# Performance work log

Hardware: AMD Instinct MI355X
Metric: run time of the kernel (lower is better)

Reference implementation:

```python
import jax, jax.numpy as jnp
import numpy as np

RPN_BATCHSIZE = 256
RPN_FG_FRACTION = 0.5
NEG_OVERLAP = 0.3
POS_OVERLAP = 0.7
STRIDE = 16
ALLOWED_BORDER = 0.0


def _whctrs(a):
    w = a[2] - a[0] + 1.0
    h = a[3] - a[1] + 1.0
    return w, h, a[0] + 0.5 * (w - 1.0), a[1] + 0.5 * (h - 1.0)


def _mkanchors(ws, hs, xc, yc):
    return np.stack([xc - 0.5 * (ws - 1.0), yc - 0.5 * (hs - 1.0),
                     xc + 0.5 * (ws - 1.0), yc + 0.5 * (hs - 1.0)], axis=1)


def _base_anchors(base_size=16, ratios=(0.5, 1.0, 2.0), scales=(8.0, 16.0, 32.0)):
    ratios = np.asarray(ratios, np.float64)
    scales = np.asarray(scales, np.float64)
    base = np.array([1.0, 1.0, base_size, base_size]) - 1.0
    w, h, xc, yc = _whctrs(base)
    size = w * h
    ws = np.round(np.sqrt(size / ratios))
    hs = np.round(ws * ratios)
    ratio_anchors = _mkanchors(ws, hs, xc, yc)
    out = []
    for ra in ratio_anchors:
        w2, h2, xc2, yc2 = _whctrs(ra)
        out.append(_mkanchors(w2 * scales, h2 * scales, xc2, yc2))
    return np.concatenate(out, axis=0).astype(np.float32)  # (9, 4)


def _shift_anchors(rr, cc, stride):
    base = jnp.asarray(_base_anchors())  # (9, 4)
    sx = jnp.arange(rr, dtype=jnp.float32) * stride
    sy = jnp.arange(cc, dtype=jnp.float32) * stride
    SX, SY = jnp.meshgrid(sx, sy)  # 'xy' indexing like keras meshgrid
    shifts = jnp.stack([SX.ravel(), SY.ravel(), SX.ravel(), SY.ravel()], axis=1)
    return (base[None, :, :] + shifts[:, None, :]).reshape(-1, 4)  # (rr*cc*9, 4)


def _overlap(a, b):
    # pairwise IoU with the +1 pixel convention of keras_rcnn.backend.overlap
    area_a = (a[:, 2] - a[:, 0] + 1.0) * (a[:, 3] - a[:, 1] + 1.0)  # (N,)
    area_b = (b[:, 2] - b[:, 0] + 1.0) * (b[:, 3] - b[:, 1] + 1.0)  # (G,)
    iw = jnp.maximum(jnp.minimum(a[:, None, 2], b[None, :, 2]) - jnp.maximum(a[:, None, 0], b[None, :, 0]) + 1.0, 0.0)
    ih = jnp.maximum(jnp.minimum(a[:, None, 3], b[None, :, 3]) - jnp.maximum(a[:, None, 1], b[None, :, 1]) + 1.0, 0.0)
    inter = iw * ih
    return inter / (area_a[:, None] + area_b[None, :] - inter)


def _subsample(labels, target_value, max_count, key):
    # Randomly demote entries with labels == target_value beyond max_count to -1.
    # Replaces the TF shuffle+scatter with a vectorized rank-based selection.
    is_t = labels == target_value
    pri = jnp.where(is_t, jax.random.uniform(key, labels.shape), -1.0)
    order = jnp.argsort(-pri)
    n = labels.shape[0]
    rank = jnp.zeros((n,), jnp.int32).at[order].set(jnp.arange(n, dtype=jnp.int32))
    drop = is_t & (rank >= max_count)
    return jnp.where(drop, -1.0, labels)


def _bbox_transform(ex, gt):
    ew = ex[:, 2] - ex[:, 0] + 1.0
    eh = ex[:, 3] - ex[:, 1] + 1.0
    ecx = ex[:, 0] + 0.5 * ew
    ecy = ex[:, 1] + 0.5 * eh
    gw = gt[:, 2] - gt[:, 0] + 1.0
    gh = gt[:, 3] - gt[:, 1] + 1.0
    gcx = gt[:, 0] + 0.5 * gw
    gcy = gt[:, 1] + 0.5 * gh
    dx = (gcx - ecx) / ew
    dy = (gcy - ecy) / eh
    dw = jnp.log(gw / ew)
    dh = jnp.log(gh / eh)
    return jnp.stack([dx, dy, dw, dh], axis=1)


def _forward(scores, gt_boxes, metadata):
    meta = metadata[0]
    gt = gt_boxes[0]
    rr, cc = scores.shape[1], scores.shape[2]
    anchors = _shift_anchors(rr, cc, STRIDE)
    n = anchors.shape[0]
    iou = _overlap(anchors, gt)  # (N, G), dominant memory traffic
    argmax_inds = jnp.argmax(iou, axis=1)        # best gt per anchor
    max_overlaps = jnp.max(iou, axis=1)
    gt_argmax_inds = jnp.argmax(iou, axis=0)     # best anchor per gt
    labels = jnp.full((n,), -1.0, jnp.float32)
    labels = jnp.where(max_overlaps < NEG_OVERLAP, 0.0, labels)
    # unique+scatter_add in the original just sets those positions to 1
    labels = labels.at[gt_argmax_inds].set(1.0)
    labels = jnp.where(max_overlaps >= POS_OVERLAP, 1.0, labels)
    kpos, kneg = jax.random.split(jax.random.key(42))
    num_fg = int(RPN_FG_FRACTION * RPN_BATCHSIZE)
    labels = _subsample(labels, 1.0, num_fg, kpos)
    num_bg = RPN_BATCHSIZE - jnp.sum(labels == 1.0)
    labels = _subsample(labels, 0.0, num_bg, kneg)
    gt_sel = gt[argmax_inds]  # (N, 4)
    targets = _bbox_transform(anchors, gt_sel)
    inside = ((anchors[:, 0] >= -ALLOWED_BORDER) & (anchors[:, 1] >= -ALLOWED_BORDER) &
              (anchors[:, 2] < ALLOWED_BORDER + meta[1]) & (anchors[:, 3] < ALLOWED_BORDER + meta[0]))
    labels = jnp.where(inside, labels, -1.0)
    return labels[None, :], targets[None, :, :]


def setup_inputs() -> dict:
    key = jax.random.key(0)
    k1, k2 = jax.random.split(key)
    rr = cc = 128
    num_anchors = 9
    g = 256
    scores = jnp.zeros((1, rr, cc, 2 * num_anchors), jnp.float32)
    xy1 = jax.random.uniform(k1, (g, 2), jnp.float32) * 1600.0
    wh = 32.0 + jax.random.uniform(k2, (g, 2), jnp.float32) * 416.0
    xy2 = jnp.minimum(xy1 + wh, 2047.0)
    gt_boxes = jnp.concatenate([xy1, xy2], axis=1)[None, :, :]
    metadata = jnp.array([[2048.0, 2048.0, 1.0]], jnp.float32)
    return {"scores": scores, "gt_boxes": gt_boxes, "metadata": metadata}


def reference(scores, gt_boxes, metadata):
    return _forward(scores, gt_boxes, metadata)
```

## Files before the change

kernel.cpp:

```cpp
#include <hip/hip_runtime.h>
#include <stdint.h>

#pragma clang fp contract(off)

#define N_ANCH 147456
#define HALF_N 73728u
#define NG 256
#define NBINS 4096
#define CAND_CAP 4096
#define K_POS 128u
#define RPN_BATCH 256u
#define PARTITIONABLE 1

struct TFOut { uint32_t x0, x1; };

__host__ __device__ constexpr TFOut threefry2x32(uint32_t k0, uint32_t k1,
                                                 uint32_t c0, uint32_t c1) {
  uint32_t ks[3] = {k0, k1, k0 ^ k1 ^ 0x1BD11BDAu};
  uint32_t x0 = c0 + ks[0];
  uint32_t x1 = c1 + ks[1];
  const uint32_t rotA[4] = {13u, 15u, 26u, 6u};
  const uint32_t rotB[4] = {17u, 29u, 16u, 24u};
#pragma unroll
  for (int g = 0; g < 5; ++g) {
#pragma unroll
    for (int r = 0; r < 4; ++r) {
      uint32_t ro = ((g & 1) == 0) ? rotA[r] : rotB[r];
      x0 += x1;
      x1 = (x1 << ro) | (x1 >> (32u - ro));
      x1 ^= x0;
    }
    x0 += ks[(g + 1) % 3];
    x1 += ks[(g + 2) % 3] + (uint32_t)(g + 1);
  }
  return TFOut{x0, x1};
}

#if PARTITIONABLE
constexpr TFOut SK0 = threefry2x32(0u, 42u, 0u, 0u);
constexpr TFOut SK1 = threefry2x32(0u, 42u, 0u, 1u);
constexpr uint32_t KPOS0 = SK0.x0, KPOS1 = SK0.x1;
constexpr uint32_t KNEG0 = SK1.x0, KNEG1 = SK1.x1;
#else
constexpr TFOut SA = threefry2x32(0u, 42u, 0u, 2u);
constexpr TFOut SB = threefry2x32(0u, 42u, 1u, 3u);
constexpr uint32_t KPOS0 = SA.x0, KPOS1 = SB.x0;
constexpr uint32_t KNEG0 = SA.x1, KNEG1 = SB.x1;
#endif

__device__ __forceinline__ uint32_t rand_m23(uint32_t k0, uint32_t k1, uint32_t i) {
#if PARTITIONABLE
  TFOut o = threefry2x32(k0, k1, 0u, i);
  return (o.x0 ^ o.x1) >> 9;
#else
  uint32_t lo = (i < HALF_N) ? i : i - HALF_N;
  TFOut o = threefry2x32(k0, k1, lo, lo + HALF_N);
  return ((i < HALF_N) ? o.x0 : o.x1) >> 9;
#endif
}

__device__ const float c_base[9][4] = {
  { -84.f,  -40.f,  99.f,  55.f}, {-176.f,  -88.f, 191.f, 103.f},
  {-360.f, -184.f, 375.f, 199.f}, { -56.f,  -56.f,  71.f,  71.f},
  {-120.f, -120.f, 135.f, 135.f}, {-248.f, -248.f, 263.f, 263.f},
  { -36.f,  -80.f,  51.f,  95.f}, { -80.f, -168.f,  95.f, 183.f},
  {-168.f, -344.f, 183.f, 359.f}
};

__device__ __forceinline__ void anchor_coords(int a, float* x1, float* y1,
                                              float* x2, float* y2) {
  int b = a % 9;
  int cell = a / 9;
  float sx = (float)((cell & 127) << 4);
  float sy = (float)((cell >> 7) << 4);
  *x1 = c_base[b][0] + sx;
  *y1 = c_base[b][1] + sy;
  *x2 = c_base[b][2] + sx;
  *y2 = c_base[b][3] + sy;
}

__global__ __launch_bounds__(256) void k_anchor(const float* __restrict__ gt,
                                                float* __restrict__ labels,
                                                float* __restrict__ targets,
                                                uint32_t* __restrict__ hp,
                                                uint32_t* __restrict__ hn) {
  __shared__ float4 s_gt[NG];
  __shared__ float s_area[NG];
  const int tid = threadIdx.x;
  float4 bb = ((const float4*)gt)[tid];
  s_gt[tid] = bb;
  s_area[tid] = (bb.z - bb.x + 1.0f) * (bb.w - bb.y + 1.0f);
  __syncthreads();
  const int a = blockIdx.x * 256 + tid;
  float ax1, ay1, ax2, ay2;
  anchor_coords(a, &ax1, &ay1, &ax2, &ay2);
  const float area_a = (ax2 - ax1 + 1.0f) * (ay2 - ay1 + 1.0f);

  unsigned long long c0 = 0x00000000FFFFFFFFull;
  unsigned long long c1 = 0ull, c2 = 0ull, c3 = 0ull;
#define IOU_STEP(JJ, CH)                                                  \
  {                                                                       \
    float4 b = s_gt[(JJ)];                                                \
    float iw = fminf(ax2, b.z) - fmaxf(ax1, b.x) + 1.0f;                  \
    float ih = fminf(ay2, b.w) - fmaxf(ay1, b.y) + 1.0f;                  \
    if (iw > 0.0f && ih > 0.0f) {                                         \
      float inter = iw * ih;                                              \
      float v = inter / (area_a + s_area[(JJ)] - inter);                  \
      unsigned long long key =                                            \
          ((unsigned long long)__float_as_uint(v) << 32)                  \
        | (unsigned long long)(0xFFFFFFFFu - (uint32_t)(JJ));             \
      if (key > CH) CH = key;                                             \
    }                                                                     \
  }
  for (int j = 0; j < NG; j += 4) {
    IOU_STEP(j + 0, c0)
    IOU_STEP(j + 1, c1)
    IOU_STEP(j + 2, c2)
    IOU_STEP(j + 3, c3)
  }
#undef IOU_STEP
  if (c1 > c0) c0 = c1;
  if (c2 > c0) c0 = c2;
  if (c3 > c0) c0 = c3;
  const float best = __uint_as_float((uint32_t)(c0 >> 32));
  const int bj = (int)(0xFFFFFFFFu - (uint32_t)c0);

  float l = (best >= 0.7f) ? 1.0f : ((best < 0.3f) ? 0.0f : -1.0f);
  labels[a] = l;
  if (l == 1.0f) {
    atomicAdd(&hp[rand_m23(KPOS0, KPOS1, (uint32_t)a) >> 11], 1u);
  } else if (l == 0.0f) {
    atomicAdd(&hn[rand_m23(KNEG0, KNEG1, (uint32_t)a) >> 11], 1u);
  }

  float4 g = s_gt[bj];
  float ew = ax2 - ax1 + 1.0f;
  float eh = ay2 - ay1 + 1.0f;
  float ecx = ax1 + 0.5f * ew;
  float ecy = ay1 + 0.5f * eh;
  float gw = g.z - g.x + 1.0f;
  float gh = g.w - g.y + 1.0f;
  float gcx = g.x + 0.5f * gw;
  float gcy = g.y + 0.5f * gh;
  float4 t;
  t.x = (gcx - ecx) / ew;
  t.y = (gcy - ecy) / eh;
  t.z = logf(gw / ew);
  t.w = logf(gh / eh);
  ((float4*)targets)[a] = t;
}

__global__ __launch_bounds__(256) void k_gtbest_sep(const float* __restrict__ gt,
                                                    float* __restrict__ labels,
                                                    uint32_t* __restrict__ hp,
                                                    uint32_t* __restrict__ hn) {
  __shared__ unsigned long long s_best[2][9];
  __shared__ unsigned long long s_k[9];
  const int j = blockIdx.x;
  const int tid = threadIdx.x;
  if (tid < 18) s_best[tid / 9][tid % 9] = 0ull;
  __syncthreads();
  float4 b = ((const float4*)gt)[j];
  const int axis = tid >> 7;
  const int p = tid & 127;
  const float shift = (float)(p << 4);
  const float lo = axis ? b.y : b.x;
  const float hi = axis ? b.w : b.z;
#pragma unroll
  for (int k = 0; k < 9; ++k) {
    const float a1 = c_base[k][axis] + shift;
    const float a2 = c_base[k][axis + 2] + shift;
    float ext = fminf(a2, hi) - fmaxf(a1, lo) + 1.0f;
    ext = fmaxf(ext, 0.0f);
    unsigned long long key =
        ((unsigned long long)__float_as_uint(ext) << 7)
      | (unsigned long long)(127 - p);
    atomicMax(&s_best[axis][k], key);
  }
  __syncthreads();
  if (tid < 9) {
    const int k = tid;
    unsigned long long kx = s_best[0][k], ky = s_best[1][k];
    float iw = __uint_as_float((uint32_t)(kx >> 7));
    float ih = __uint_as_float((uint32_t)(ky >> 7));
    int xs = 127 - (int)(kx & 127u);
    int ys = 127 - (int)(ky & 127u);
    float inter = iw * ih;
    float area_a = (c_base[k][2] - c_base[k][0] + 1.0f) *
                   (c_base[k][3] - c_base[k][1] + 1.0f);
    float area_b = (b.z - b.x + 1.0f) * (b.w - b.y + 1.0f);
    float v = inter / (area_a + area_b - inter);
    uint32_t a = (uint32_t)((ys * 128 + xs) * 9 + k);
    s_k[k] = ((unsigned long long)__float_as_uint(v) << 32)
           | (unsigned long long)(0xFFFFFFFFu - a);
  }
  __syncthreads();
  if (tid == 0) {
    unsigned long long best = s_k[0];
#pragma unroll
    for (int k = 1; k < 9; ++k) if (s_k[k] > best) best = s_k[k];
    uint32_t besta = 0xFFFFFFFFu - (uint32_t)(best & 0xFFFFFFFFull);
    float old = atomicExch(&labels[besta], 1.0f);
    if (old == 0.0f) {
      atomicSub(&hn[rand_m23(KNEG0, KNEG1, besta) >> 11], 1u);
      atomicAdd(&hp[rand_m23(KPOS0, KPOS1, besta) >> 11], 1u);
    } else if (old == -1.0f) {
      atomicAdd(&hp[rand_m23(KPOS0, KPOS1, besta) >> 11], 1u);
    }
  }
}

__global__ __launch_bounds__(1024) void k_findbin(const uint32_t* __restrict__ hp,
                                                  const uint32_t* __restrict__ hn,
                                                  uint32_t* __restrict__ ctrl) {
  __shared__ uint32_t s_h[NBINS];
  __shared__ uint32_t s_c[64];
  __shared__ uint32_t s_kneg;
  const int tid = threadIdx.x;

  for (int i = tid; i < NBINS; i += 1024) s_h[i] = hp[i];
  __syncthreads();
  if (tid < 64) {
    uint32_t s = 0;
    for (int i = 0; i < 64; ++i) s += s_h[tid * 64 + i];
    s_c[tid] = s;
  }
  __syncthreads();
  if (tid == 0) {
    uint32_t total = 0;
    for (int i = 0; i < 64; ++i) total += s_c[i];
    if (total <= K_POS) {
      ctrl[0] = 0u;
      s_kneg = RPN_BATCH - total;
    } else {
      uint32_t cum = 0; int ch, bb;
      for (ch = 63; ch >= 0; --ch) { if (cum + s_c[ch] >= K_POS) break; cum += s_c[ch]; }
      for (bb = ch * 64 + 63; bb >= ch * 64; --bb) { if (cum + s_h[bb] >= K_POS) break; cum += s_h[bb]; }
      ctrl[0] = 1u; ctrl[1] = (uint32_t)bb; ctrl[2] = K_POS - cum;
      s_kneg = RPN_BATCH - K_POS;
    }
  }
  __syncthreads();
  for (int i = tid; i < NBINS; i += 1024) s_h[i] = hn[i];
  __syncthreads();
  if (tid < 64) {
    uint32_t s = 0;
    for (int i = 0; i < 64; ++i) s += s_h[tid * 64 + i];
    s_c[tid] = s;
  }
  __syncthreads();
  if (tid == 0) {
    uint32_t total = 0;
    for (int i = 0; i < 64; ++i) total += s_c[i];
    uint32_t K = s_kneg;
    if (K == 0u) {
      ctrl[4] = 0u;
      ((unsigned long long*)ctrl)[5] = ~0ull;
    } else if (total <= K) {
      ctrl[4] = 0u;
    } else {
      uint32_t cum = 0; int ch, bb;
      for (ch = 63; ch >= 0; --ch) { if (cum + s_c[ch] >= K) break; cum += s_c[ch]; }
      for (bb = ch * 64 + 63; bb >= ch * 64; --bb) { if (cum + s_h[bb] >= K) break; cum += s_h[bb]; }
      ctrl[4] = 1u; ctrl[5] = (uint32_t)bb; ctrl[6] = K - cum;
    }
  }
}

__global__ __launch_bounds__(256) void k_collect(const float* __restrict__ labels,
                                                 uint32_t* __restrict__ ctrl,
                                                 unsigned long long* __restrict__ cp,
                                                 unsigned long long* __restrict__ cn) {
  const int a = blockIdx.x * 256 + threadIdx.x;
  float l = labels[a];
  if (l == 1.0f) {
    if (ctrl[0]) {
      uint32_t m = rand_m23(KPOS0, KPOS1, (uint32_t)a);
      if ((m >> 11) == ctrl[1]) {
        uint32_t i = atomicAdd(&ctrl[3], 1u);
        if (i < CAND_CAP)
          cp[i] = ((unsigned long long)m << 32) | (unsigned long long)(0xFFFFFFFFu - (uint32_t)a);
      }
    }
  } else if (l == 0.0f) {
    if (ctrl[4]) {
      uint32_t m = rand_m23(KNEG0, KNEG1, (uint32_t)a);
      if ((m >> 11) == ctrl[5]) {
        uint32_t i = atomicAdd(&ctrl[7], 1u);
        if (i < CAND_CAP)
          cn[i] = ((unsigned long long)m << 32) | (unsigned long long)(0xFFFFFFFFu - (uint32_t)a);
      }
    }
  }
}

__global__ __launch_bounds__(1024) void k_cutoff(uint32_t* __restrict__ ctrl,
                                                 const unsigned long long* __restrict__ cp,
                                                 const unsigned long long* __restrict__ cn) {
  __shared__ unsigned long long s_k[CAND_CAP];
  __shared__ unsigned long long s_m[1024];
  const int tid = threadIdx.x;
  for (int phase = 0; phase < 2; ++phase) {
    uint32_t active = ctrl[phase ? 4 : 0];
    if (!active) continue;
    uint32_t c = ctrl[phase ? 7 : 3];
    if (c > CAND_CAP) c = CAND_CAP;
    uint32_t need = ctrl[phase ? 6 : 2];
    const unsigned long long* cand = phase ? cn : cp;
    for (uint32_t i = tid; i < c; i += 1024) s_k[i] = cand[i];
    __syncthreads();
    unsigned long long mymin = ~0ull;
    for (uint32_t i = tid; i < c; i += 1024) {
      unsigned long long k = s_k[i];
      uint32_t r = 0;
      for (uint32_t j = 0; j < c; ++j) r += (s_k[j] > k) ? 1u : 0u;
      if (r < need && k < mymin) mymin = k;
    }
    s_m[tid] = mymin;
    __syncthreads();
    for (int s = 512; s > 0; s >>= 1) {
      if (tid < s) {
        unsigned long long o = s_m[tid + s];
        if (o < s_m[tid]) s_m[tid] = o;
      }
      __syncthreads();
    }
    if (tid == 0) ((unsigned long long*)ctrl)[4 + phase] = s_m[0];
    __syncthreads();
  }
}

__global__ __launch_bounds__(256) void k_apply(float* __restrict__ labels,
                                               const float* __restrict__ meta,
                                               const uint32_t* __restrict__ ctrl) {
  const int a = blockIdx.x * 256 + threadIdx.x;
  float l = labels[a];
  const unsigned long long* cut = (const unsigned long long*)ctrl;
  if (l == 1.0f) {
    unsigned long long key = ((unsigned long long)rand_m23(KPOS0, KPOS1, (uint32_t)a) << 32)
                           | (unsigned long long)(0xFFFFFFFFu - (uint32_t)a);
    if (key < cut[4]) l = -1.0f;
  } else if (l == 0.0f) {
    unsigned long long key = ((unsigned long long)rand_m23(KNEG0, KNEG1, (uint32_t)a) << 32)
                           | (unsigned long long)(0xFFFFFFFFu - (uint32_t)a);
    if (key < cut[5]) l = -1.0f;
  }
  float x1, y1, x2, y2;
  anchor_coords(a, &x1, &y1, &x2, &y2);
  float hh = meta[0], ww = meta[1];
  bool inside = (x1 >= 0.0f) && (y1 >= 0.0f) && (x2 < ww) && (y2 < hh);
  if (!inside) l = -1.0f;
  labels[a] = l;
}

extern "C" void kernel_launch(void* const* d_in, const int* in_sizes, int n_in,
                              void* d_out, int out_size, void* d_ws, size_t ws_size,
                              hipStream_t stream) {
  (void)in_sizes; (void)n_in; (void)out_size; (void)ws_size;
  const float* gt   = (const float*)d_in[1];
  const float* meta = (const float*)d_in[2];
  float* labels  = (float*)d_out;
  float* targets = labels + N_ANCH;

  uint8_t* ws = (uint8_t*)d_ws;
  uint32_t* hp   = (uint32_t*)(ws);
  uint32_t* hn   = (uint32_t*)(ws + 16384);
  uint32_t* ctrl = (uint32_t*)(ws + 32768);
  unsigned long long* cp = (unsigned long long*)(ws + 32896);
  unsigned long long* cn = (unsigned long long*)(ws + 32896 + 32768);

  hipMemsetAsync(d_ws, 0, 32896, stream);
  k_anchor     <<<N_ANCH / 256, 256, 0, stream>>>(gt, labels, targets, hp, hn);
  k_gtbest_sep <<<NG, 256, 0, stream>>>(gt, labels, hp, hn);
  k_findbin    <<<1, 1024, 0, stream>>>(hp, hn, ctrl);
  k_collect    <<<N_ANCH / 256, 256, 0, stream>>>(labels, ctrl, cp, cn);
  k_cutoff     <<<1, 1024, 0, stream>>>(ctrl, cp, cn);
  k_apply      <<<N_ANCH / 256, 256, 0, stream>>>(labels, meta, ctrl);
}
```

Baseline: 110.1 us.

## Fuse all stages into one cooperative kernel with grid-wide syncs

Replaces the memset plus six separate kernel launches with a single cooperative kernel of 576 blocks that uses grid.sync between phases. Workspace zeroing and the per-gt best-anchor search run in the first phase, then IoU/targets, histogram bin finding, candidate collection, cutoff ranking and label application, with single-block phases done by block 0. This removes launch overhead and inter-kernel gaps, at the cost of five grid barriers, idle blocks during serial phases, and block 0 doing the cutoff ranking with 256 instead of 1024 threads.

Result: slower. 403.3 us (+266.4%).

```diff
diff --git a/kernel.cpp b/kernel.cpp
--- a/kernel.cpp
+++ b/kernel.cpp
@@ -1,16 +1,18 @@
 #include <hip/hip_runtime.h>
+#include <hip/hip_cooperative_groups.h>
 #include <stdint.h>
 
+namespace cg = cooperative_groups;
+
 #pragma clang fp contract(off)
 
 #define N_ANCH 147456
-#define HALF_N 73728u
+#define NBLK 576
 #define NG 256
 #define NBINS 4096
 #define CAND_CAP 4096
 #define K_POS 128u
 #define RPN_BATCH 256u
-#define PARTITIONABLE 1
 
 struct TFOut { uint32_t x0, x1; };
 
@@ -36,27 +38,14 @@
   return TFOut{x0, x1};
 }
 
-#if PARTITIONABLE
 constexpr TFOut SK0 = threefry2x32(0u, 42u, 0u, 0u);
 constexpr TFOut SK1 = threefry2x32(0u, 42u, 0u, 1u);
 constexpr uint32_t KPOS0 = SK0.x0, KPOS1 = SK0.x1;
 constexpr uint32_t KNEG0 = SK1.x0, KNEG1 = SK1.x1;
-#else
-constexpr TFOut SA = threefry2x32(0u, 42u, 0u, 2u);
-constexpr TFOut SB = threefry2x32(0u, 42u, 1u, 3u);
-constexpr uint32_t KPOS0 = SA.x0, KPOS1 = SB.x0;
-constexpr uint32_t KNEG0 = SA.x1, KNEG1 = SB.x1;
-#endif
 
 __device__ __forceinline__ uint32_t rand_m23(uint32_t k0, uint32_t k1, uint32_t i) {
-#if PARTITIONABLE
   TFOut o = threefry2x32(k0, k1, 0u, i);
   return (o.x0 ^ o.x1) >> 9;
-#else
-  uint32_t lo = (i < HALF_N) ? i : i - HALF_N;
-  TFOut o = threefry2x32(k0, k1, lo, lo + HALF_N);
-  return ((i < HALF_N) ? o.x0 : o.x1) >> 9;
-#endif
 }
 
 __device__ const float c_base[9][4] = {
@@ -79,23 +68,90 @@
   *y2 = c_base[b][3] + sy;
 }
 
-__global__ __launch_bounds__(256) void k_anchor(const float* __restrict__ gt,
-                                                float* __restrict__ labels,
-                                                float* __restrict__ targets,
-                                                uint32_t* __restrict__ hp,
-                                                uint32_t* __restrict__ hn) {
-  __shared__ float4 s_gt[NG];
-  __shared__ float s_area[NG];
+
+__global__ __launch_bounds__(256) void k_fused(const float* __restrict__ gt,
+                                               const float* __restrict__ meta,
+                                               float* __restrict__ labels,
+                                               float* __restrict__ targets,
+                                               uint8_t* __restrict__ ws) {
+  uint32_t* wsw  = (uint32_t*)ws;
+  uint32_t* hp   = wsw;
+  uint32_t* hn   = wsw + 4096;
+  uint32_t* ctrl = wsw + 8192;
+  uint32_t* gl   = wsw + 8224;
+  unsigned long long* cut = (unsigned long long*)ctrl;
+  unsigned long long* cp  = (unsigned long long*)(ws + 33920);
+  unsigned long long* cn  = (unsigned long long*)(ws + 66688);
+
+  __shared__ unsigned long long smem[4352];
   const int tid = threadIdx.x;
-  float4 bb = ((const float4*)gt)[tid];
-  s_gt[tid] = bb;
-  s_area[tid] = (bb.z - bb.x + 1.0f) * (bb.w - bb.y + 1.0f);
+  const int bid = blockIdx.x;
+  cg::grid_group grid = cg::this_grid();
+
+  if (bid >= NG) {
+    int w = (bid - NG) * 256 + tid;
+    if (w < 8224) wsw[w] = 0u;
+  } else {
+    unsigned long long* s_best = smem;
+    unsigned long long* s_kk   = smem + 18;
+    if (tid < 18) s_best[tid] = 0ull;
+    __syncthreads();
+    float4 b = ((const float4*)gt)[bid];
+    const int axis = tid >> 7;
+    const int p = tid & 127;
+    const float shift = (float)(p << 4);
+    const float lo = axis ? b.y : b.x;
+    const float hi = axis ? b.w : b.z;
+#pragma unroll
+    for (int k = 0; k < 9; ++k) {
+      float a1 = c_base[k][axis] + shift;
+      float a2 = c_base[k][axis + 2] + shift;
+      float ext = fminf(a2, hi) - fmaxf(a1, lo) + 1.0f;
+      ext = fmaxf(ext, 0.0f);
+      unsigned long long key =
+          ((unsigned long long)__float_as_uint(ext) << 7)
+        | (unsigned long long)(127 - p);
+      atomicMax(&s_best[axis * 9 + k], key);
+    }
+    __syncthreads();
+    if (tid < 9) {
+      const int k = tid;
+      unsigned long long kx = s_best[k], ky = s_best[9 + k];
+      float iw = __uint_as_float((uint32_t)(kx >> 7));
+      float ih = __uint_as_float((uint32_t)(ky >> 7));
+      int xs = 127 - (int)(kx & 127u);
+      int ys = 127 - (int)(ky & 127u);
+      float inter = iw * ih;
+      float area_a = (c_base[k][2] - c_base[k][0] + 1.0f) *
+                     (c_base[k][3] - c_base[k][1] + 1.0f);
+      float area_b = (b.z - b.x + 1.0f) * (b.w - b.y + 1.0f);
+      float v = inter / (area_a + area_b - inter);
+      uint32_t a = (uint32_t)((ys * 128 + xs) * 9 + k);
+      s_kk[k] = ((unsigned long long)__float_as_uint(v) << 32)
+              | (unsigned long long)(0xFFFFFFFFu - a);
+    }
+    __syncthreads();
+    if (tid == 0) {
+      unsigned long long best = s_kk[0];
+#pragma unroll
+      for (int k = 1; k < 9; ++k) if (s_kk[k] > best) best = s_kk[k];
+      gl[bid] = 0xFFFFFFFFu - (uint32_t)(best & 0xFFFFFFFFull);
+    }
+  }
+  grid.sync();
+
+  float4* s_gt  = (float4*)smem;
+  float*  s_area = (float*)((char*)smem + 4096);
+  {
+    float4 bb = ((const float4*)gt)[tid];
+    s_gt[tid] = bb;
+    s_area[tid] = (bb.z - bb.x + 1.0f) * (bb.w - bb.y + 1.0f);
+  }
   __syncthreads();
-  const int a = blockIdx.x * 256 + tid;
+  const int a = bid * 256 + tid;
   float ax1, ay1, ax2, ay2;
   anchor_coords(a, &ax1, &ay1, &ax2, &ay2);
   const float area_a = (ax2 - ax1 + 1.0f) * (ay2 - ay1 + 1.0f);
-
   unsigned long long c0 = 0x00000000FFFFFFFFull;
   unsigned long long c1 = 0ull, c2 = 0ull, c3 = 0ull;
 #define IOU_STEP(JJ, CH)                                                  \
@@ -124,155 +180,98 @@
   if (c3 > c0) c0 = c3;
   const float best = __uint_as_float((uint32_t)(c0 >> 32));
   const int bj = (int)(0xFFFFFFFFu - (uint32_t)c0);
-
-  float l = (best >= 0.7f) ? 1.0f : ((best < 0.3f) ? 0.0f : -1.0f);
-  labels[a] = l;
-  if (l == 1.0f) {
+  float l0 = (best >= 0.7f) ? 1.0f : ((best < 0.3f) ? 0.0f : -1.0f);
+  labels[a] = l0;
+  if (l0 == 1.0f) {
     atomicAdd(&hp[rand_m23(KPOS0, KPOS1, (uint32_t)a) >> 11], 1u);
-  } else if (l == 0.0f) {
+  } else if (l0 == 0.0f) {
     atomicAdd(&hn[rand_m23(KNEG0, KNEG1, (uint32_t)a) >> 11], 1u);
   }
-
-  float4 g = s_gt[bj];
-  float ew = ax2 - ax1 + 1.0f;
-  float eh = ay2 - ay1 + 1.0f;
-  float ecx = ax1 + 0.5f * ew;
-  float ecy = ay1 + 0.5f * eh;
-  float gw = g.z - g.x + 1.0f;
-  float gh = g.w - g.y + 1.0f;
-  float gcx = g.x + 0.5f * gw;
-  float gcy = g.y + 0.5f * gh;
-  float4 t;
-  t.x = (gcx - ecx) / ew;
-  t.y = (gcy - ecy) / eh;
-  t.z = logf(gw / ew);
-  t.w = logf(gh / eh);
-  ((float4*)targets)[a] = t;
-}
-
-__global__ __launch_bounds__(256) void k_gtbest_sep(const float* __restrict__ gt,
-                                                    float* __restrict__ labels,
-                                                    uint32_t* __restrict__ hp,
-                                                    uint32_t* __restrict__ hn) {
-  __shared__ unsigned long long s_best[2][9];
-  __shared__ unsigned long long s_k[9];
-  const int j = blockIdx.x;
-  const int tid = threadIdx.x;
-  if (tid < 18) s_best[tid / 9][tid % 9] = 0ull;
-  __syncthreads();
-  float4 b = ((const float4*)gt)[j];
-  const int axis = tid >> 7;
-  const int p = tid & 127;
-  const float shift = (float)(p << 4);
-  const float lo = axis ? b.y : b.x;
-  const float hi = axis ? b.w : b.z;
-#pragma unroll
-  for (int k = 0; k < 9; ++k) {
-    const float a1 = c_base[k][axis] + shift;
-    const float a2 = c_base[k][axis + 2] + shift;
-    float ext = fminf(a2, hi) - fmaxf(a1, lo) + 1.0f;
-    ext = fmaxf(ext, 0.0f);
-    unsigned long long key =
-        ((unsigned long long)__float_as_uint(ext) << 7)
-      | (unsigned long long)(127 - p);
-    atomicMax(&s_best[axis][k], key);
-  }
-  __syncthreads();
-  if (tid < 9) {
-    const int k = tid;
-    unsigned long long kx = s_best[0][k], ky = s_best[1][k];
-    float iw = __uint_as_float((uint32_t)(kx >> 7));
-    float ih = __uint_as_float((uint32_t)(ky >> 7));
-    int xs = 127 - (int)(kx & 127u);
-    int ys = 127 - (int)(ky & 127u);
-    float inter = iw * ih;
-    float area_a = (c_base[k][2] - c_base[k][0] + 1.0f) *
-                   (c_base[k][3] - c_base[k][1] + 1.0f);
-    float area_b = (b.z - b.x + 1.0f) * (b.w - b.y + 1.0f);
-    float v = inter / (area_a + area_b - inter);
-    uint32_t a = (uint32_t)((ys * 128 + xs) * 9 + k);
-    s_k[k] = ((unsigned long long)__float_as_uint(v) << 32)
-           | (unsigned long long)(0xFFFFFFFFu - a);
-  }
-  __syncthreads();
-  if (tid == 0) {
-    unsigned long long best = s_k[0];
-#pragma unroll
-    for (int k = 1; k < 9; ++k) if (s_k[k] > best) best = s_k[k];
-    uint32_t besta = 0xFFFFFFFFu - (uint32_t)(best & 0xFFFFFFFFull);
-    float old = atomicExch(&labels[besta], 1.0f);
-    if (old == 0.0f) {
-      atomicSub(&hn[rand_m23(KNEG0, KNEG1, besta) >> 11], 1u);
-      atomicAdd(&hp[rand_m23(KPOS0, KPOS1, besta) >> 11], 1u);
-    } else if (old == -1.0f) {
-      atomicAdd(&hp[rand_m23(KPOS0, KPOS1, besta) >> 11], 1u);
-    }
-  }
-}
-
-__global__ __launch_bounds__(1024) void k_findbin(const uint32_t* __restrict__ hp,
-                                                  const uint32_t* __restrict__ hn,
-                                                  uint32_t* __restrict__ ctrl) {
-  __shared__ uint32_t s_h[NBINS];
-  __shared__ uint32_t s_c[64];
-  __shared__ uint32_t s_kneg;
-  const int tid = threadIdx.x;
-
-  for (int i = tid; i < NBINS; i += 1024) s_h[i] = hp[i];
-  __syncthreads();
-  if (tid < 64) {
-    uint32_t s = 0;
-    for (int i = 0; i < 64; ++i) s += s_h[tid * 64 + i];
-    s_c[tid] = s;
-  }
-  __syncthreads();
-  if (tid == 0) {
-    uint32_t total = 0;
-    for (int i = 0; i < 64; ++i) total += s_c[i];
-    if (total <= K_POS) {
-      ctrl[0] = 0u;
-      s_kneg = RPN_BATCH - total;
-    } else {
-      uint32_t cum = 0; int ch, bb;
-      for (ch = 63; ch >= 0; --ch) { if (cum + s_c[ch] >= K_POS) break; cum += s_c[ch]; }
-      for (bb = ch * 64 + 63; bb >= ch * 64; --bb) { if (cum + s_h[bb] >= K_POS) break; cum += s_h[bb]; }
-      ctrl[0] = 1u; ctrl[1] = (uint32_t)bb; ctrl[2] = K_POS - cum;
-      s_kneg = RPN_BATCH - K_POS;
-    }
-  }
-  __syncthreads();
-  for (int i = tid; i < NBINS; i += 1024) s_h[i] = hn[i];
-  __syncthreads();
-  if (tid < 64) {
-    uint32_t s = 0;
-    for (int i = 0; i < 64; ++i) s += s_h[tid * 64 + i];
-    s_c[tid] = s;
-  }
-  __syncthreads();
-  if (tid == 0) {
-    uint32_t total = 0;
-    for (int i = 0; i < 64; ++i) total += s_c[i];
-    uint32_t K = s_kneg;
-    if (K == 0u) {
-      ctrl[4] = 0u;
-      ((unsigned long long*)ctrl)[5] = ~0ull;
-    } else if (total <= K) {
-      ctrl[4] = 0u;
-    } else {
-      uint32_t cum = 0; int ch, bb;
-      for (ch = 63; ch >= 0; --ch) { if (cum + s_c[ch] >= K) break; cum += s_c[ch]; }
-      for (bb = ch * 64 + 63; bb >= ch * 64; --bb) { if (cum + s_h[bb] >= K) break; cum += s_h[bb]; }
-      ctrl[4] = 1u; ctrl[5] = (uint32_t)bb; ctrl[6] = K - cum;
-    }
-  }
-}
-
-__global__ __launch_bounds__(256) void k_collect(const float* __restrict__ labels,
-                                                 uint32_t* __restrict__ ctrl,
-                                                 unsigned long long* __restrict__ cp,
-                                                 unsigned long long* __restrict__ cn) {
-  const int a = blockIdx.x * 256 + threadIdx.x;
-  float l = labels[a];
+  {
+    float4 g = s_gt[bj];
+    float ew = ax2 - ax1 + 1.0f;
+    float eh = ay2 - ay1 + 1.0f;
+    float ecx = ax1 + 0.5f * ew;
+    float ecy = ay1 + 0.5f * eh;
+    float gw = g.z - g.x + 1.0f;
+    float gh = g.w - g.y + 1.0f;
+    float gcx = g.x + 0.5f * gw;
+    float gcy = g.y + 0.5f * gh;
+    float4 t;
+    t.x = (gcx - ecx) / ew;
+    t.y = (gcy - ecy) / eh;
+    t.z = logf(gw / ew);
+    t.w = logf(gh / eh);
+    ((float4*)targets)[a] = t;
+  }
+  grid.sync();
+
+  if (bid == 0) {
+    {
+      uint32_t g = gl[tid];
+      float old = atomicExch(&labels[g], 1.0f);
+      if (old == 0.0f) {
+        atomicSub(&hn[rand_m23(KNEG0, KNEG1, g) >> 11], 1u);
+        atomicAdd(&hp[rand_m23(KPOS0, KPOS1, g) >> 11], 1u);
+      } else if (old == -1.0f) {
+        atomicAdd(&hp[rand_m23(KPOS0, KPOS1, g) >> 11], 1u);
+      }
+    }
+    __syncthreads();
+    uint32_t* s_h = (uint32_t*)smem;
+    uint32_t* s_c = (uint32_t*)smem + NBINS;
+    __shared__ uint32_t s_kneg;
+    for (int i = tid; i < NBINS; i += 256) s_h[i] = hp[i];
+    __syncthreads();
+    if (tid < 64) {
+      uint32_t s = 0;
+      for (int i = 0; i < 64; ++i) s += s_h[tid * 64 + i];
+      s_c[tid] = s;
+    }
+    __syncthreads();
+    if (tid == 0) {
+      uint32_t total = 0;
+      for (int i = 0; i < 64; ++i) total += s_c[i];
+      if (total <= K_POS) {
+        ctrl[0] = 0u;
+        s_kneg = RPN_BATCH - total;
+      } else {
+        uint32_t cum = 0; int ch, bb;
+        for (ch = 63; ch >= 0; --ch) { if (cum + s_c[ch] >= K_POS) break; cum += s_c[ch]; }
+        for (bb = ch * 64 + 63; bb >= ch * 64; --bb) { if (cum + s_h[bb] >= K_POS) break; cum += s_h[bb]; }
+        ctrl[0] = 1u; ctrl[1] = (uint32_t)bb; ctrl[2] = K_POS - cum;
+        s_kneg = RPN_BATCH - K_POS;
+      }
+    }
+    __syncthreads();
+    for (int i = tid; i < NBINS; i += 256) s_h[i] = hn[i];
+    __syncthreads();
+    if (tid < 64) {
+      uint32_t s = 0;
+      for (int i = 0; i < 64; ++i) s += s_h[tid * 64 + i];
+      s_c[tid] = s;
+    }
+    __syncthreads();
+    if (tid == 0) {
+      uint32_t total = 0;
+      for (int i = 0; i < 64; ++i) total += s_c[i];
+      uint32_t K = s_kneg;
+      if (K == 0u) {
+        ctrl[4] = 0u;
+        cut[5] = ~0ull;
+      } else if (total <= K) {
+        ctrl[4] = 0u;
+      } else {
+        uint32_t cum = 0; int ch, bb;
+        for (ch = 63; ch >= 0; --ch) { if (cum + s_c[ch] >= K) break; cum += s_c[ch]; }
+        for (bb = ch * 64 + 63; bb >= ch * 64; --bb) { if (cum + s_h[bb] >= K) break; cum += s_h[bb]; }
+        ctrl[4] = 1u; ctrl[5] = (uint32_t)bb; ctrl[6] = K - cum;
+      }
+    }
+  }
+  grid.sync();
+
+  const float l = __hip_atomic_load(&labels[a], __ATOMIC_RELAXED, __HIP_MEMORY_SCOPE_AGENT);
   if (l == 1.0f) {
     if (ctrl[0]) {
       uint32_t m = rand_m23(KPOS0, KPOS1, (uint32_t)a);
@@ -292,65 +291,59 @@
       }
     }
   }
-}
-
-__global__ __launch_bounds__(1024) void k_cutoff(uint32_t* __restrict__ ctrl,
-                                                 const unsigned long long* __restrict__ cp,
-                                                 const unsigned long long* __restrict__ cn) {
-  __shared__ unsigned long long s_k[CAND_CAP];
-  __shared__ unsigned long long s_m[1024];
-  const int tid = threadIdx.x;
-  for (int phase = 0; phase < 2; ++phase) {
-    uint32_t active = ctrl[phase ? 4 : 0];
-    if (!active) continue;
-    uint32_t c = ctrl[phase ? 7 : 3];
-    if (c > CAND_CAP) c = CAND_CAP;
-    uint32_t need = ctrl[phase ? 6 : 2];
-    const unsigned long long* cand = phase ? cn : cp;
-    for (uint32_t i = tid; i < c; i += 1024) s_k[i] = cand[i];
-    __syncthreads();
-    unsigned long long mymin = ~0ull;
-    for (uint32_t i = tid; i < c; i += 1024) {
-      unsigned long long k = s_k[i];
-      uint32_t r = 0;
-      for (uint32_t j = 0; j < c; ++j) r += (s_k[j] > k) ? 1u : 0u;
-      if (r < need && k < mymin) mymin = k;
-    }
-    s_m[tid] = mymin;
-    __syncthreads();
-    for (int s = 512; s > 0; s >>= 1) {
-      if (tid < s) {
-        unsigned long long o = s_m[tid + s];
-        if (o < s_m[tid]) s_m[tid] = o;
-      }
+  grid.sync();
+
+  if (bid == 0) {
+    unsigned long long* s_k = smem;
+    unsigned long long* s_m = smem + CAND_CAP;
+    for (int phase = 0; phase < 2; ++phase) {
+      uint32_t active = __hip_atomic_load(&ctrl[phase ? 4 : 0], __ATOMIC_RELAXED, __HIP_MEMORY_SCOPE_AGENT);
+      if (!active) continue;
+      uint32_t c = __hip_atomic_load(&ctrl[phase ? 7 : 3], __ATOMIC_RELAXED, __HIP_MEMORY_SCOPE_AGENT);
+      if (c > CAND_CAP) c = CAND_CAP;
+      uint32_t need = __hip_atomic_load(&ctrl[phase ? 6 : 2], __ATOMIC_RELAXED, __HIP_MEMORY_SCOPE_AGENT);
+      const unsigned long long* cand = phase ? cn : cp;
+      for (uint32_t i = tid; i < c; i += 256) s_k[i] = cand[i];
       __syncthreads();
-    }
-    if (tid == 0) ((unsigned long long*)ctrl)[4 + phase] = s_m[0];
-    __syncthreads();
-  }
-}
-
-__global__ __launch_bounds__(256) void k_apply(float* __restrict__ labels,
-                                               const float* __restrict__ meta,
-                                               const uint32_t* __restrict__ ctrl) {
-  const int a = blockIdx.x * 256 + threadIdx.x;
-  float l = labels[a];
-  const unsigned long long* cut = (const unsigned long long*)ctrl;
-  if (l == 1.0f) {
+      unsigned long long mymin = ~0ull;
+      for (uint32_t i = tid; i < c; i += 256) {
+        unsigned long long k = s_k[i];
+        uint32_t r = 0;
+        for (uint32_t j = 0; j < c; ++j) r += (s_k[j] > k) ? 1u : 0u;
+        if (r < need && k < mymin) mymin = k;
+      }
+      s_m[tid] = mymin;
+      __syncthreads();
+      for (int s = 128; s > 0; s >>= 1) {
+        if (tid < s) {
+          unsigned long long o = s_m[tid + s];
+          if (o < s_m[tid]) s_m[tid] = o;
+        }
+        __syncthreads();
+      }
+      if (tid == 0)
+        __hip_atomic_store(&cut[4 + phase], s_m[0], __ATOMIC_RELAXED, __HIP_MEMORY_SCOPE_AGENT);
+      __syncthreads();
+    }
+  }
+  grid.sync();
+
+  float lf = l;
+  if (lf == 1.0f) {
     unsigned long long key = ((unsigned long long)rand_m23(KPOS0, KPOS1, (uint32_t)a) << 32)
                            | (unsigned long long)(0xFFFFFFFFu - (uint32_t)a);
-    if (key < cut[4]) l = -1.0f;
-  } else if (l == 0.0f) {
+    if (key < __hip_atomic_load(&cut[4], __ATOMIC_RELAXED, __HIP_MEMORY_SCOPE_AGENT)) lf = -1.0f;
+  } else if (lf == 0.0f) {
     unsigned long long key = ((unsigned long long)rand_m23(KNEG0, KNEG1, (uint32_t)a) << 32)
                            | (unsigned long long)(0xFFFFFFFFu - (uint32_t)a);
-    if (key < cut[5]) l = -1.0f;
-  }
-  float x1, y1, x2, y2;
-  anchor_coords(a, &x1, &y1, &x2, &y2);
-  float hh = meta[0], ww = meta[1];
-  bool inside = (x1 >= 0.0f) && (y1 >= 0.0f) && (x2 < ww) && (y2 < hh);
-  if (!inside) l = -1.0f;
-  labels[a] = l;
+    if (key < __hip_atomic_load(&cut[5], __ATOMIC_RELAXED, __HIP_MEMORY_SCOPE_AGENT)) lf = -1.0f;
+  }
+  {
+    float hh = meta[0], ww = meta[1];
+    bool inside = (ax1 >= 0.0f) && (ay1 >= 0.0f) && (ax2 < ww) && (ay2 < hh);
+    if (!inside) lf = -1.0f;
+  }
+  labels[a] = lf;
 }
 
 extern "C" void kernel_launch(void* const* d_in, const int* in_sizes, int n_in,
@@ -361,19 +354,9 @@
   const float* meta = (const float*)d_in[2];
   float* labels  = (float*)d_out;
   float* targets = labels + N_ANCH;
-
   uint8_t* ws = (uint8_t*)d_ws;
-  uint32_t* hp   = (uint32_t*)(ws);
-  uint32_t* hn   = (uint32_t*)(ws + 16384);
-  uint32_t* ctrl = (uint32_t*)(ws + 32768);
-  unsigned long long* cp = (unsigned long long*)(ws + 32896);
-  unsigned long long* cn = (unsigned long long*)(ws + 32896 + 32768);
-
-  hipMemsetAsync(d_ws, 0, 32896, stream);
-  k_anchor     <<<N_ANCH / 256, 256, 0, stream>>>(gt, labels, targets, hp, hn);
-  k_gtbest_sep <<<NG, 256, 0, stream>>>(gt, labels, hp, hn);
-  k_findbin    <<<1, 1024, 0, stream>>>(hp, hn, ctrl);
-  k_collect    <<<N_ANCH / 256, 256, 0, stream>>>(labels, ctrl, cp, cn);
-  k_cutoff     <<<1, 1024, 0, stream>>>(ctrl, cp, cn);
-  k_apply      <<<N_ANCH / 256, 256, 0, stream>>>(labels, meta, ctrl);
-}
+
+  void* args[] = {(void*)&gt, (void*)&meta, (void*)&labels, (void*)&targets, (void*)&ws};
+  hipLaunchCooperativeKernel((const void*)k_fused, dim3(NBLK), dim3(256),
+                             args, 0, stream);
+}
```
